# Kernel tuning notes

Hardware: AMD Instinct MI355X
Metric: run time of the kernel (lower is better)

## Reference

```python
import jax, jax.numpy as jnp
import numpy as np

B, T, D, H, C = 128, 1024, 128, 256, 128


def _kaiming(key, shape):
    # torch kaiming_normal_ (fan_in = shape[1] for these (in,out) matrices)
    std = np.sqrt(2.0 / shape[1]).astype(np.float32)
    return jax.random.normal(key, shape, dtype=jnp.float32) * std


def setup_inputs() -> dict:
    key = jax.random.key(0)
    ks = jax.random.split(key, 10)
    return {
        "x": jax.random.normal(ks[0], (B, T, D), dtype=jnp.float32),
        "w_gx": _kaiming(ks[1], (D, H)), "w_gh": _kaiming(ks[2], (H, H)), "b_g": jnp.zeros((H,), jnp.float32),
        "w_ix": _kaiming(ks[3], (D, H)), "w_ih": _kaiming(ks[4], (H, H)), "b_i": jnp.zeros((H,), jnp.float32),
        "w_fx": _kaiming(ks[5], (D, H)), "w_fh": _kaiming(ks[6], (H, H)), "b_f": jnp.zeros((H,), jnp.float32),
        "w_ox": _kaiming(ks[7], (D, H)), "w_oh": _kaiming(ks[8], (H, H)), "b_o": jnp.zeros((H,), jnp.float32),
        "w_ph": _kaiming(ks[9], (H, C)), "b_p": jnp.zeros((C,), jnp.float32),
    }


def reference(x, w_gx, w_gh, b_g, w_ix, w_ih, b_i, w_fx, w_fh, b_f,
              w_ox, w_oh, b_o, w_ph, b_p):
    # Stack the 4 gate projections into single GEMMs (same math, fused).
    w_x = jnp.concatenate([w_gx, w_ix, w_fx, w_ox], axis=1)  # [D, 4H]
    w_h = jnp.concatenate([w_gh, w_ih, w_fh, w_oh], axis=1)  # [H, 4H]
    b = jnp.concatenate([b_g, b_i, b_f, b_o])                # [4H]

    # Precompute input projections for all timesteps: [T, B, 4H]
    xproj = jnp.einsum('btd,dk->tbk', x, w_x) + b

    h0 = jnp.zeros((x.shape[0], w_gh.shape[0]), x.dtype)
    c0 = jnp.zeros_like(h0)

    def step(carry, xp_t):
        h, c = carry
        gates = xp_t + h @ w_h                      # [B, 4H]
        g, i, f, o = jnp.split(gates, 4, axis=1)
        g = jnp.tanh(g)
        i = jax.nn.sigmoid(i)
        f = jax.nn.sigmoid(f)
        o = jax.nn.sigmoid(o)
        c = g * i + c * f
        h = jnp.tanh(c) * o
        return (h, c), None

    (h_T, _), _ = jax.lax.scan(step, (h0, c0), xproj)
    # Original computes p_t every step but returns only the last one.
    return h_T @ w_ph + b_p
```

## Files before the change

### kernel.cpp

```cpp
#include <hip/hip_runtime.h>

typedef __attribute__((ext_vector_type(8))) short short8;
typedef __attribute__((ext_vector_type(4))) short short4_t;
typedef __attribute__((ext_vector_type(4))) float f32x4;

#define LOG2E 1.44269504088896340736f

static __device__ __forceinline__ unsigned short f2bf(float f) {
  unsigned int u = __builtin_bit_cast(unsigned int, f);
  u += 0x7fffu + ((u >> 16) & 1u);
  return (unsigned short)(u >> 16);
}
static __device__ __forceinline__ float bf2f(unsigned short h) {
  return __builtin_bit_cast(float, ((unsigned int)h) << 16);
}
static __device__ __forceinline__ f32x4 mfma16(short8 a, short8 b, f32x4 c) {
  return __builtin_amdgcn_mfma_f32_16x16x32_bf16(a, b, c, 0, 0, 0);
}
static __device__ __forceinline__ f32x4 cvt4(short4_t v) {
  f32x4 o;
  o[0] = bf2f((unsigned short)v[0]); o[1] = bf2f((unsigned short)v[1]);
  o[2] = bf2f((unsigned short)v[2]); o[3] = bf2f((unsigned short)v[3]);
  return o;
}
static __device__ __forceinline__ f32x4 sig4(f32x4 v) {
  f32x4 o;
#pragma unroll
  for (int r = 0; r < 4; ++r)
    o[r] = __builtin_amdgcn_rcpf(1.0f + __builtin_amdgcn_exp2f(-v[r]));
  return o;
}
static __device__ __forceinline__ f32x4 tanh4(f32x4 v) {
  f32x4 o;
#pragma unroll
  for (int r = 0; r < 4; ++r)
    o[r] = 2.0f * __builtin_amdgcn_rcpf(1.0f + __builtin_amdgcn_exp2f(-v[r])) - 1.0f;
  return o;
}

__global__ __launch_bounds__(256) void pack_kernel(
    const float* __restrict__ w_gx, const float* __restrict__ w_gh, const float* __restrict__ b_g,
    const float* __restrict__ w_ix, const float* __restrict__ w_ih, const float* __restrict__ b_i,
    const float* __restrict__ w_fx, const float* __restrict__ w_fh, const float* __restrict__ b_f,
    const float* __restrict__ w_ox, const float* __restrict__ w_oh, const float* __restrict__ b_o,
    const float* __restrict__ w_ph,
    short* __restrict__ pwh, short* __restrict__ pwx, short* __restrict__ pwph,
    float* __restrict__ bsc)
{
  int e = blockIdx.x * 256 + threadIdx.x;
  if (e < 262144) {
    int j = e & 7, l = (e >> 3) & 63, tf = e >> 9;
    int kk = tf & 7, n = (tf >> 3) & 1, g = (tf >> 4) & 3, w = tf >> 6;
    int q = l >> 4, rr = l & 15;
    int k = 32 * kk + 8 * q + j;
    int col = 32 * w + 16 * n + rr;
    const float* wh = (g == 0) ? w_gh : (g == 1) ? w_ih : (g == 2) ? w_fh : w_oh;
    float s = (g == 0) ? 2.0f * LOG2E : LOG2E;
    pwh[e] = (short)f2bf(wh[k * 256 + col] * s);
  } else if (e < 262144 + 131072) {
    int e2 = e - 262144;
    int j = e2 & 7, l = (e2 >> 3) & 63, kk = (e2 >> 9) & 3, ct = e2 >> 11;
    int q = l >> 4, rr = l & 15;
    int g = ct >> 4;
    int colg = (ct & 15) * 16 + rr;
    int k = 32 * kk + 8 * q + j;
    const float* wx = (g == 0) ? w_gx : (g == 1) ? w_ix : (g == 2) ? w_fx : w_ox;
    float s = (g == 0) ? 2.0f * LOG2E : LOG2E;
    pwx[e2] = (short)f2bf(wx[k * 256 + colg] * s);
  } else if (e < 262144 + 131072 + 32768) {
    int e3 = e - (262144 + 131072);
    int j = e3 & 7, l = (e3 >> 3) & 63, kk = (e3 >> 9) & 7, tc = e3 >> 12;
    int q = l >> 4, rr = l & 15;
    int k = 32 * kk + 8 * q + j;
    int col = tc * 16 + rr;
    pwph[e3] = (short)f2bf(w_ph[k * 128 + col]);
  } else if (e < 262144 + 131072 + 32768 + 1024) {
    int e4 = e - (262144 + 131072 + 32768);
    int g = e4 >> 8, c = e4 & 255;
    const float* bb = (g == 0) ? b_g : (g == 1) ? b_i : (g == 2) ? b_f : b_o;
    float s = (g == 0) ? 2.0f * LOG2E : LOG2E;
    bsc[e4] = bb[c] * s;
  }
}

__global__ __launch_bounds__(256) void xproj_kernel(
    const float* __restrict__ x, const short* __restrict__ pwx,
    const float* __restrict__ bsc, short* __restrict__ xp, int t0)
{
  __shared__ short xt[2048];
  int tid = threadIdx.x;
  int tloc = blockIdx.x, gb = blockIdx.y;
  int t = t0 + tloc;
  {
    int r = tid >> 4, dg = tid & 15;
    const float* src = x + ((size_t)(gb * 16 + r) * 1024 + t) * 128 + dg * 8;
    f32x4 u0 = *(const f32x4*)src;
    f32x4 u1 = *(const f32x4*)(src + 4);
    short8 v;
    v[0] = (short)f2bf(u0[0]); v[1] = (short)f2bf(u0[1]);
    v[2] = (short)f2bf(u0[2]); v[3] = (short)f2bf(u0[3]);
    v[4] = (short)f2bf(u1[0]); v[5] = (short)f2bf(u1[1]);
    v[6] = (short)f2bf(u1[2]); v[7] = (short)f2bf(u1[3]);
    *(short8*)((char*)xt + r * 256 + ((dg * 16) ^ ((r & 7) << 4))) = v;
  }
  __syncthreads();
  int wv = tid >> 6, lane = tid & 63;
  int q = lane >> 4, rr = lane & 15;
  short8 a[4];
#pragma unroll
  for (int kk = 0; kk < 4; ++kk)
    a[kk] = *(const short8*)((const char*)xt + rr * 256 + ((kk * 64 + q * 16) ^ ((rr & 7) << 4)));
#pragma unroll
  for (int i = 0; i < 16; ++i) {
    int ct = wv * 16 + i;
    float bias = bsc[ct * 16 + rr];
    f32x4 acc = {bias, bias, bias, bias};
#pragma unroll
    for (int kk = 0; kk < 4; ++kk) {
      short8 b = *(const short8*)(pwx + (size_t)(ct * 4 + kk) * 512 + lane * 8);
      acc = mfma16(a[kk], b, acc);
    }
    int wrec = (ct >> 1) & 7, tt2 = (ct >> 4) * 2 + (ct & 1);
    short4_t o;
    o[0] = (short)f2bf(acc[0]); o[1] = (short)f2bf(acc[1]);
    o[2] = (short)f2bf(acc[2]); o[3] = (short)f2bf(acc[3]);
    *(short4_t*)(xp + ((size_t)(tloc * 8 + gb) * 64 + wrec * 8 + tt2) * 256 + lane * 4) = o;
  }
}

__global__ __launch_bounds__(512, 2) void rec_kernel(
    const short* __restrict__ pwh, const short* __restrict__ xp,
    const short* __restrict__ pwph, const float* __restrict__ b_p,
    float* __restrict__ state_c, short* __restrict__ state_h,
    float* __restrict__ out, int tlen, int first, int last)
{
  __shared__ char lds[147456];
  int tid = threadIdx.x;
  int gb = blockIdx.x;
  int w = tid >> 6, lane = tid & 63;
  int q = lane >> 4, rr = lane & 15;
  char* hb = lds;

  f32x4 cst0, cst1;
  if (first) {
    f32x4 z = {0.f, 0.f, 0.f, 0.f};
    cst0 = z; cst1 = z;
    short8 z8 = {0, 0, 0, 0, 0, 0, 0, 0};
    *(short8*)(hb + tid * 16) = z8;
  } else {
    cst0 = *(const f32x4*)(state_c + ((size_t)(gb * 8 + w) * 2 + 0) * 256 + lane * 4);
    cst1 = *(const f32x4*)(state_c + ((size_t)(gb * 8 + w) * 2 + 1) * 256 + lane * 4);
#pragma unroll
    for (int n = 0; n < 2; ++n) {
      short4_t hs = *(const short4_t*)(state_h + ((size_t)(gb * 8 + w) * 2 + n) * 256 + lane * 4);
#pragma unroll
      for (int r = 0; r < 4; ++r) {
        int row = q * 4 + r, col = 32 * w + 16 * n + rr;
        *(short*)(hb + row * 512 + ((col * 2) ^ ((row & 7) << 4))) = hs[r];
      }
    }
  }
  {
    int lf = tid >> 2, part = tid & 3;
    int ww = lf >> 4, tt = (lf >> 3) & 1, kk = lf & 7;
    const short* src = pwh + (size_t)((ww * 8 + tt) * 8 + kk) * 512 + part * 128;
    short8* dst = (short8*)(lds + 16384 + (size_t)lf * 1024 + part * 256);
#pragma unroll
    for (int i = 0; i < 16; ++i) dst[i] = ((const short8*)src)[i];
  }
  __syncthreads();

  const short* wbase = pwh + (size_t)w * 64 * 512 + lane * 8;
  const char* gw = lds + 16384 + (size_t)(w * 2) * 8192 + lane * 16;

  const short* xpbase = xp + (size_t)gb * 64 * 256 + (w * 8) * 256 + lane * 4;
  short4_t xpc[8];
#pragma unroll
  for (int tt = 0; tt < 8; ++tt)
    xpc[tt] = *(const short4_t*)(xpbase + (size_t)tt * 256);

  unsigned par = 0;
  for (int t = 0; t < tlen; ++t) {
    short8 a[8];
#pragma unroll
    for (int kk = 0; kk < 8; ++kk)
      a[kk] = *(const short8*)(hb + par * 8192 + rr * 512 + ((kk * 64 + q * 16) ^ ((rr & 7) << 4)));
    short8 sA[2][8];
#pragma unroll
    for (int t2 = 0; t2 < 2; ++t2)
#pragma unroll
      for (int kk = 0; kk < 8; ++kk)
        sA[t2][kk] = *(const short8*)(wbase + (size_t)((t2 + 2) * 8 + kk) * 512);
    short4_t xpn[8];
    {
      int tn = (t + 1 < tlen) ? (t + 1) : t;
      const short* xpnb = xp + ((size_t)tn * 8 + gb) * 64 * 256 + (w * 8) * 256 + lane * 4;
#pragma unroll
      for (int tt = 0; tt < 8; ++tt)
        xpn[tt] = *(const short4_t*)(xpnb + (size_t)tt * 256);
    }

    f32x4 aG0 = cvt4(xpc[0]), aG1 = cvt4(xpc[1]);
#pragma unroll
    for (int kk = 0; kk < 8; ++kk) {
      short8 w0 = *(const short8*)(gw + (size_t)kk * 1024);
      short8 w1 = *(const short8*)(gw + 8192 + (size_t)kk * 1024);
      aG0 = mfma16(a[kk], w0, aG0);
      aG1 = mfma16(a[kk], w1, aG1);
    }
    short8 sB[2][8];
#pragma unroll
    for (int t2 = 0; t2 < 2; ++t2)
#pragma unroll
      for (int kk = 0; kk < 8; ++kk)
        sB[t2][kk] = *(const short8*)(wbase + (size_t)((t2 + 4) * 8 + kk) * 512);
    f32x4 tg0 = tanh4(aG0), tg1 = tanh4(aG1);

    f32x4 aI0 = cvt4(xpc[2]), aI1 = cvt4(xpc[3]);
#pragma unroll
    for (int kk = 0; kk < 8; ++kk) {
      aI0 = mfma16(a[kk], sA[0][kk], aI0);
      aI1 = mfma16(a[kk], sA[1][kk], aI1);
    }
#pragma unroll
    for (int t2 = 0; t2 < 2; ++t2)
#pragma unroll
      for (int kk = 0; kk < 8; ++kk)
        sA[t2][kk] = *(const short8*)(wbase + (size_t)((t2 + 6) * 8 + kk) * 512);
    f32x4 p0, p1;
    {
      f32x4 si0 = sig4(aI0), si1 = sig4(aI1);
#pragma unroll
      for (int r = 0; r < 4; ++r) { p0[r] = tg0[r] * si0[r]; p1[r] = tg1[r] * si1[r]; }
    }

    f32x4 aF0 = cvt4(xpc[4]), aF1 = cvt4(xpc[5]);
#pragma unroll
    for (int kk = 0; kk < 8; ++kk) {
      aF0 = mfma16(a[kk], sB[0][kk], aF0);
      aF1 = mfma16(a[kk], sB[1][kk], aF1);
    }
    {
      f32x4 sf0 = sig4(aF0), sf1 = sig4(aF1);
#pragma unroll
      for (int r = 0; r < 4; ++r) {
        cst0[r] = p0[r] + cst0[r] * sf0[r];
        cst1[r] = p1[r] + cst1[r] * sf1[r];
      }
    }

    f32x4 aO0 = cvt4(xpc[6]), aO1 = cvt4(xpc[7]);
#pragma unroll
    for (int kk = 0; kk < 8; ++kk) {
      aO0 = mfma16(a[kk], sA[0][kk], aO0);
      aO1 = mfma16(a[kk], sA[1][kk], aO1);
    }
    {
      f32x4 so0 = sig4(aO0), so1 = sig4(aO1);
      f32x4 c2s0, c2s1;
#pragma unroll
      for (int r = 0; r < 4; ++r) { c2s0[r] = 2.0f * LOG2E * cst0[r]; c2s1[r] = 2.0f * LOG2E * cst1[r]; }
      f32x4 th0 = tanh4(c2s0), th1 = tanh4(c2s1);
#pragma unroll
      for (int r = 0; r < 4; ++r) {
        int row = q * 4 + r;
        int col0 = 32 * w + rr, col1 = 32 * w + 16 + rr;
        *(short*)(hb + (par ^ 1) * 8192 + row * 512 + ((col0 * 2) ^ ((row & 7) << 4))) =
            (short)f2bf(th0[r] * so0[r]);
        *(short*)(hb + (par ^ 1) * 8192 + row * 512 + ((col1 * 2) ^ ((row & 7) << 4))) =
            (short)f2bf(th1[r] * so1[r]);
      }
    }
    __syncthreads();
    par ^= 1;
#pragma unroll
    for (int tt = 0; tt < 8; ++tt) xpc[tt] = xpn[tt];
  }

  if (!last) {
    *(f32x4*)(state_c + ((size_t)(gb * 8 + w) * 2 + 0) * 256 + lane * 4) = cst0;
    *(f32x4*)(state_c + ((size_t)(gb * 8 + w) * 2 + 1) * 256 + lane * 4) = cst1;
#pragma unroll
    for (int n = 0; n < 2; ++n) {
      short4_t hs;
#pragma unroll
      for (int r = 0; r < 4; ++r) {
        int row = q * 4 + r, col = 32 * w + 16 * n + rr;
        hs[r] = *(const short*)(hb + par * 8192 + row * 512 + ((col * 2) ^ ((row & 7) << 4)));
      }
      *(short4_t*)(state_h + ((size_t)(gb * 8 + w) * 2 + n) * 256 + lane * 4) = hs;
    }
  } else {
    float bias = b_p[w * 16 + rr];
    f32x4 po = {bias, bias, bias, bias};
#pragma unroll
    for (int kk = 0; kk < 8; ++kk) {
      short8 a2 = *(const short8*)(hb + par * 8192 + rr * 512 + ((kk * 64 + q * 16) ^ ((rr & 7) << 4)));
      short8 b = *(const short8*)(pwph + (size_t)(w * 8 + kk) * 512 + lane * 8);
      po = mfma16(a2, b, po);
    }
#pragma unroll
    for (int r = 0; r < 4; ++r)
      out[(size_t)(gb * 16 + q * 4 + r) * 128 + w * 16 + rr] = po[r];
  }
}

extern "C" void kernel_launch(void* const* d_in, const int* in_sizes, int n_in,
                              void* d_out, int out_size, void* d_ws, size_t ws_size,
                              hipStream_t stream) {
  const float* x    = (const float*)d_in[0];
  const float* w_gx = (const float*)d_in[1];
  const float* w_gh = (const float*)d_in[2];
  const float* b_g  = (const float*)d_in[3];
  const float* w_ix = (const float*)d_in[4];
  const float* w_ih = (const float*)d_in[5];
  const float* b_i  = (const float*)d_in[6];
  const float* w_fx = (const float*)d_in[7];
  const float* w_fh = (const float*)d_in[8];
  const float* b_f  = (const float*)d_in[9];
  const float* w_ox = (const float*)d_in[10];
  const float* w_oh = (const float*)d_in[11];
  const float* b_o  = (const float*)d_in[12];
  const float* w_ph = (const float*)d_in[13];
  const float* b_p  = (const float*)d_in[14];

  char* ws = (char*)d_ws;
  short* pwh  = (short*)(ws);
  short* pwx  = (short*)(ws + 524288);
  short* pwph = (short*)(ws + 786432);
  float* bsc  = (float*)(ws + 851968);
  float* stc  = (float*)(ws + 856064);
  short* sth  = (short*)(ws + 987136);
  short* xp   = (short*)(ws + 1052672);

  size_t avail = (ws_size > 1052672) ? (ws_size - 1052672) : 0;
  int Tc = 1024;
  while (Tc > 1 && (size_t)Tc * 262144 > avail) Tc >>= 1;

  pack_kernel<<<1668, 256, 0, stream>>>(w_gx, w_gh, b_g, w_ix, w_ih, b_i,
                                        w_fx, w_fh, b_f, w_ox, w_oh, b_o,
                                        w_ph, pwh, pwx, pwph, bsc);
  for (int t0 = 0; t0 < 1024; t0 += Tc) {
    xproj_kernel<<<dim3(Tc, 8), 256, 0, stream>>>(x, pwx, bsc, xp, t0);
    rec_kernel<<<dim3(8), 512, 0, stream>>>(pwh, xp, pwph, b_p, stc, sth,
                                            (float*)d_out, Tc, t0 == 0 ? 1 : 0,
                                            (t0 + Tc == 1024) ? 1 : 0);
  }
  (void)in_sizes; (void)n_in; (void)out_size;
}
```

Baseline: 2.783 ms.

## Keep input-gate weights in registers and reorder gate computation in LSTM loop

Loads the input-gate recurrent weight fragments into registers once before the time loop instead of reloading them from global memory every step. Reorders per-step work to G, F, I, O so only the forget and output weights are streamed each step through one shared register buffer. Only the next step's G-gate input projection is prefetched; the other gates' projections are loaded at the start of the current step. This cuts per-step global weight traffic and register pressure from the double-buffered projections, at the cost of less latency hiding for the non-G projection loads.

```diff
diff --git a/kernel.cpp b/kernel.cpp
--- a/kernel.cpp
+++ b/kernel.cpp
@@ -173,34 +173,38 @@
   const short* wbase = pwh + (size_t)w * 64 * 512 + lane * 8;
   const char* gw = lds + 16384 + (size_t)(w * 2) * 8192 + lane * 16;
 
+  short8 sI[2][8];
+#pragma unroll
+  for (int t2 = 0; t2 < 2; ++t2)
+#pragma unroll
+    for (int kk = 0; kk < 8; ++kk)
+      sI[t2][kk] = *(const short8*)(wbase + (size_t)((t2 + 2) * 8 + kk) * 512);
+
   const short* xpbase = xp + (size_t)gb * 64 * 256 + (w * 8) * 256 + lane * 4;
-  short4_t xpc[8];
-#pragma unroll
-  for (int tt = 0; tt < 8; ++tt)
-    xpc[tt] = *(const short4_t*)(xpbase + (size_t)tt * 256);
+  short4_t xg0 = *(const short4_t*)(xpbase + 0 * 256);
+  short4_t xg1 = *(const short4_t*)(xpbase + 1 * 256);
 
   unsigned par = 0;
   for (int t = 0; t < tlen; ++t) {
+    const short* xpt = xp + ((size_t)t * 8 + gb) * 64 * 256 + (w * 8) * 256 + lane * 4;
     short8 a[8];
 #pragma unroll
     for (int kk = 0; kk < 8; ++kk)
       a[kk] = *(const short8*)(hb + par * 8192 + rr * 512 + ((kk * 64 + q * 16) ^ ((rr & 7) << 4)));
-    short8 sA[2][8];
+    short8 sS[2][8];
 #pragma unroll
     for (int t2 = 0; t2 < 2; ++t2)
 #pragma unroll
       for (int kk = 0; kk < 8; ++kk)
-        sA[t2][kk] = *(const short8*)(wbase + (size_t)((t2 + 2) * 8 + kk) * 512);
-    short4_t xpn[8];
-    {
-      int tn = (t + 1 < tlen) ? (t + 1) : t;
-      const short* xpnb = xp + ((size_t)tn * 8 + gb) * 64 * 256 + (w * 8) * 256 + lane * 4;
-#pragma unroll
-      for (int tt = 0; tt < 8; ++tt)
-        xpn[tt] = *(const short4_t*)(xpnb + (size_t)tt * 256);
-    }
-
-    f32x4 aG0 = cvt4(xpc[0]), aG1 = cvt4(xpc[1]);
+        sS[t2][kk] = *(const short8*)(wbase + (size_t)((t2 + 4) * 8 + kk) * 512);
+    short4_t xpi0 = *(const short4_t*)(xpt + 2 * 256);
+    short4_t xpi1 = *(const short4_t*)(xpt + 3 * 256);
+    short4_t xpf0 = *(const short4_t*)(xpt + 4 * 256);
+    short4_t xpf1 = *(const short4_t*)(xpt + 5 * 256);
+    short4_t xpo0 = *(const short4_t*)(xpt + 6 * 256);
+    short4_t xpo1 = *(const short4_t*)(xpt + 7 * 256);
+
+    f32x4 aG0 = cvt4(xg0), aG1 = cvt4(xg1);
 #pragma unroll
     for (int kk = 0; kk < 8; ++kk) {
       short8 w0 = *(const short8*)(gw + (size_t)kk * 1024);
@@ -208,52 +212,47 @@
       aG0 = mfma16(a[kk], w0, aG0);
       aG1 = mfma16(a[kk], w1, aG1);
     }
-    short8 sB[2][8];
+    f32x4 tg0 = tanh4(aG0), tg1 = tanh4(aG1);
+    {
+      int tn = (t + 1 < tlen) ? (t + 1) : t;
+      const short* xpnb = xp + ((size_t)tn * 8 + gb) * 64 * 256 + (w * 8) * 256 + lane * 4;
+      xg0 = *(const short4_t*)(xpnb + 0 * 256);
+      xg1 = *(const short4_t*)(xpnb + 1 * 256);
+    }
+
+    f32x4 aF0 = cvt4(xpf0), aF1 = cvt4(xpf1);
+#pragma unroll
+    for (int kk = 0; kk < 8; ++kk) {
+      aF0 = mfma16(a[kk], sS[0][kk], aF0);
+      aF1 = mfma16(a[kk], sS[1][kk], aF1);
+    }
+    f32x4 sf0 = sig4(aF0), sf1 = sig4(aF1);
 #pragma unroll
     for (int t2 = 0; t2 < 2; ++t2)
 #pragma unroll
       for (int kk = 0; kk < 8; ++kk)
-        sB[t2][kk] = *(const short8*)(wbase + (size_t)((t2 + 4) * 8 + kk) * 512);
-    f32x4 tg0 = tanh4(aG0), tg1 = tanh4(aG1);
-
-    f32x4 aI0 = cvt4(xpc[2]), aI1 = cvt4(xpc[3]);
-#pragma unroll
-    for (int kk = 0; kk < 8; ++kk) {
-      aI0 = mfma16(a[kk], sA[0][kk], aI0);
-      aI1 = mfma16(a[kk], sA[1][kk], aI1);
-    }
-#pragma unroll
-    for (int t2 = 0; t2 < 2; ++t2)
-#pragma unroll
-      for (int kk = 0; kk < 8; ++kk)
-        sA[t2][kk] = *(const short8*)(wbase + (size_t)((t2 + 6) * 8 + kk) * 512);
-    f32x4 p0, p1;
+        sS[t2][kk] = *(const short8*)(wbase + (size_t)((t2 + 6) * 8 + kk) * 512);
+
+    f32x4 aI0 = cvt4(xpi0), aI1 = cvt4(xpi1);
+#pragma unroll
+    for (int kk = 0; kk < 8; ++kk) {
+      aI0 = mfma16(a[kk], sI[0][kk], aI0);
+      aI1 = mfma16(a[kk], sI[1][kk], aI1);
+    }
     {
       f32x4 si0 = sig4(aI0), si1 = sig4(aI1);
 #pragma unroll
-      for (int r = 0; r < 4; ++r) { p0[r] = tg0[r] * si0[r]; p1[r] = tg1[r] * si1[r]; }
-    }
-
-    f32x4 aF0 = cvt4(xpc[4]), aF1 = cvt4(xpc[5]);
-#pragma unroll
-    for (int kk = 0; kk < 8; ++kk) {
-      aF0 = mfma16(a[kk], sB[0][kk], aF0);
-      aF1 = mfma16(a[kk], sB[1][kk], aF1);
-    }
-    {
-      f32x4 sf0 = sig4(aF0), sf1 = sig4(aF1);
-#pragma unroll
       for (int r = 0; r < 4; ++r) {
-        cst0[r] = p0[r] + cst0[r] * sf0[r];
-        cst1[r] = p1[r] + cst1[r] * sf1[r];
+        cst0[r] = tg0[r] * si0[r] + cst0[r] * sf0[r];
+        cst1[r] = tg1[r] * si1[r] + cst1[r] * sf1[r];
       }
     }
 
-    f32x4 aO0 = cvt4(xpc[6]), aO1 = cvt4(xpc[7]);
-#pragma unroll
-    for (int kk = 0; kk < 8; ++kk) {
-      aO0 = mfma16(a[kk], sA[0][kk], aO0);
-      aO1 = mfma16(a[kk], sA[1][kk], aO1);
+    f32x4 aO0 = cvt4(xpo0), aO1 = cvt4(xpo1);
+#pragma unroll
+    for (int kk = 0; kk < 8; ++kk) {
+      aO0 = mfma16(a[kk], sS[0][kk], aO0);
+      aO1 = mfma16(a[kk], sS[1][kk], aO1);
     }
     {
       f32x4 so0 = sig4(aO0), so1 = sig4(aO1);
@@ -273,8 +272,6 @@
     }
     __syncthreads();
     par ^= 1;
-#pragma unroll
-    for (int tt = 0; tt < 8; ++tt) xpc[tt] = xpn[tt];
   }
 
   if (!last) {
```

Result: slower. 4.628 ms (+66.3%).
